# Kernel optimization log

Measured on AMD Instinct MI355X. Metric: run time of the kernel, lower is better.

## Reference

```python
import jax, jax.numpy as jnp
import numpy as np

K = 2            # top-k experts
SCALING = 16.0 / 16.0  # alpha / r


def setup_inputs() -> dict:
    key = jax.random.key(0)
    ks = jax.random.split(key, 7)
    B, T, D, O, E, R = 2, 4096, 2048, 2048, 8, 16
    return {
        "x": jax.random.normal(ks[0], (B, T, D), dtype=jnp.float32),
        "W": jax.random.normal(ks[1], (O, D), dtype=jnp.float32) * (1.0 / np.sqrt(D)),
        "b": jax.random.normal(ks[2], (O,), dtype=jnp.float32) * 0.02,
        "lora_A": jax.random.normal(ks[3], (E, R, D), dtype=jnp.float32) * (1.0 / np.sqrt(D)),
        "lora_B": jax.random.normal(ks[4], (E, O, R), dtype=jnp.float32) * 0.02,
        "gate_w": jax.random.normal(ks[5], (E, D), dtype=jnp.float32) * 0.02,
        "gate_b": jax.random.normal(ks[6], (E,), dtype=jnp.float32) * 0.02,
    }


def reference(x, W, b, lora_A, lora_B, gate_w, gate_b):
    orig_shape = x.shape
    D = orig_shape[-1]
    O = W.shape[0]
    x_flat = x.reshape(-1, D)                                  # [N, D]

    base = x_flat @ W.T + b                                    # [N, O]

    logits = x_flat @ gate_w.T + gate_b                        # [N, E] (eval: no noise)
    topk_logits, topk_idx = jax.lax.top_k(logits, K)           # [N, K]
    gates = jax.nn.softmax(topk_logits, axis=-1)               # [N, K]

    xA = jnp.einsum('nd,erd->ner', x_flat, lora_A)             # [N, E, R]
    delta_all = jnp.einsum('ner,eor->neo', xA, lora_B)         # [N, E, O]

    delta_topk = jnp.take_along_axis(delta_all, topk_idx[:, :, None], axis=1)  # [N, K, O]
    lora_update = jnp.sum(delta_topk * gates[:, :, None], axis=1)              # [N, O]

    out = base + SCALING * lora_update
    return out.reshape(*orig_shape[:-1], O)
```

## Files before the change

kernel.cpp:

```cpp
#include <hip/hip_runtime.h>
#include <hip/hip_bf16.h>
#include <stdint.h>

#define N_ROWS 8192
#define DIM    2048
#define OUTD   2048
#define NEXP   8
#define RNK    16
#define ZCOLS  128
#define KAUG   2176
#define KSPLIT 4
#define KSLICE (DIM / KSPLIT)

typedef unsigned short u16;
typedef float  f32x4  __attribute__((ext_vector_type(4)));
typedef __bf16 bf16x8 __attribute__((ext_vector_type(8)));

__device__ __forceinline__ u16 f2bf(float f) {
  unsigned u = __float_as_uint(f);
  return (u16)((u + 0x7fffu + ((u >> 16) & 1u)) >> 16);
}

__global__ __launch_bounds__(256) void k1_convert_gate(
    const float* __restrict__ x, const float* __restrict__ gw,
    const float* __restrict__ gb, u16* __restrict__ xaug,
    int* __restrict__ sel, float* __restrict__ gv)
{
  const int wave = threadIdx.x >> 6;
  const int lane = threadIdx.x & 63;
  const int row0 = blockIdx.x * 8 + wave * 2;

  float xv[2][32];
  #pragma unroll
  for (int rr = 0; rr < 2; ++rr) {
    const float* xr = x + (size_t)(row0 + rr) * DIM;
    #pragma unroll
    for (int i = 0; i < 8; ++i) {
      float4 v = *(const float4*)(xr + (lane * 4 + i * 256));
      xv[rr][i*4+0] = v.x; xv[rr][i*4+1] = v.y;
      xv[rr][i*4+2] = v.z; xv[rr][i*4+3] = v.w;
    }
  }
  #pragma unroll
  for (int rr = 0; rr < 2; ++rr) {
    u16* dst = xaug + (size_t)(row0 + rr) * KAUG;
    #pragma unroll
    for (int i = 0; i < 8; ++i) {
      ushort4 s;
      s.x = f2bf(xv[rr][i*4+0]); s.y = f2bf(xv[rr][i*4+1]);
      s.z = f2bf(xv[rr][i*4+2]); s.w = f2bf(xv[rr][i*4+3]);
      *(ushort4*)(dst + (lane * 4 + i * 256)) = s;
    }
  }
  float lg[2][NEXP];
  #pragma unroll
  for (int e = 0; e < NEXP; ++e) {
    const float* ge = gw + (size_t)e * DIM;
    float s0 = 0.f, s1 = 0.f;
    #pragma unroll
    for (int i = 0; i < 8; ++i) {
      float4 g4 = *(const float4*)(ge + (lane * 4 + i * 256));
      s0 += xv[0][i*4+0]*g4.x + xv[0][i*4+1]*g4.y + xv[0][i*4+2]*g4.z + xv[0][i*4+3]*g4.w;
      s1 += xv[1][i*4+0]*g4.x + xv[1][i*4+1]*g4.y + xv[1][i*4+2]*g4.z + xv[1][i*4+3]*g4.w;
    }
    #pragma unroll
    for (int off = 32; off > 0; off >>= 1) {
      s0 += __shfl_xor(s0, off);
      s1 += __shfl_xor(s1, off);
    }
    lg[0][e] = s0 + gb[e];
    lg[1][e] = s1 + gb[e];
  }
  if (lane == 0) {
    #pragma unroll
    for (int rr = 0; rr < 2; ++rr) {
      int e0 = 0; float m0 = lg[rr][0];
      #pragma unroll
      for (int e = 1; e < NEXP; ++e) if (lg[rr][e] > m0) { m0 = lg[rr][e]; e0 = e; }
      int e1 = (e0 == 0) ? 1 : 0; float m1 = lg[rr][e1];
      #pragma unroll
      for (int e = 0; e < NEXP; ++e) if (e != e0 && lg[rr][e] > m1) { m1 = lg[rr][e]; e1 = e; }
      float t   = expf(m1 - m0);
      float inv = 1.f / (1.f + t);
      int r = row0 + rr;
      sel[2*r] = e0; sel[2*r+1] = e1;
      gv[2*r]  = inv; gv[2*r+1] = t * inv;
    }
  }
}

__global__ __launch_bounds__(256) void k2_weights(
    const float* __restrict__ W, const float* __restrict__ lB,
    const float* __restrict__ lA, u16* __restrict__ waug, u16* __restrict__ ab)
{
  const int t = threadIdx.x;
  const int bid = blockIdx.x;
  if (bid < OUTD) {
    const int o = bid;
    const float* wr = W + (size_t)o * DIM;
    u16* dst = waug + (size_t)o * KAUG;
    #pragma unroll
    for (int i = 0; i < 2; ++i) {
      int c = t * 4 + i * 1024;
      float4 v = *(const float4*)(wr + c);
      ushort4 s; s.x = f2bf(v.x); s.y = f2bf(v.y); s.z = f2bf(v.z); s.w = f2bf(v.w);
      *(ushort4*)(dst + c) = s;
    }
    if (t < ZCOLS) {
      int e = t >> 4, r = t & 15;
      dst[DIM + t] = f2bf(lB[((size_t)e * OUTD + o) * RNK + r]);
    }
  } else {
    const int ar = bid - OUTD;
    const float* src = lA + (size_t)ar * DIM;
    u16* dst = ab + (size_t)ar * DIM;
    #pragma unroll
    for (int i = 0; i < 2; ++i) {
      int c = t * 4 + i * 1024;
      float4 v = *(const float4*)(src + c);
      ushort4 s; s.x = f2bf(v.x); s.y = f2bf(v.y); s.z = f2bf(v.z); s.w = f2bf(v.w);
      *(ushort4*)(dst + c) = s;
    }
  }
}

template <int BM, int BN, int BK, int WM, int WN, int MF, int NF>
__global__ __launch_bounds__(WM*WN*64) void gemm_ksplit(
    const u16* __restrict__ A, int lda,
    const u16* __restrict__ Bm, int ldb,
    int Ksz, int gm, float* __restrict__ outP)
{
  static_assert(BM == WM * MF * 16 && BN == WN * NF * 16 && BK == 64, "geom");
  constexpr int NW   = WM * WN;
  constexpr int ROWB = BK * 2;
  __shared__ __align__(16) u16 As[2][BM * BK];
  __shared__ __align__(16) u16 Bs[2][BN * BK];

  const int wave = threadIdx.x >> 6;
  const int lane = threadIdx.x & 63;

  int bid = blockIdx.x;
  const int nwg = gridDim.x;
  if ((nwg & 7) == 0) {
    const int cpx = nwg >> 3;
    bid = (bid & 7) * cpx + (bid >> 3);
  }
  const int tm  = bid % gm;
  const int ksl = bid / gm;
  const size_t row0 = (size_t)tm * BM;
  const u16* Ak = A  + (size_t)ksl * Ksz;
  const u16* Bk = Bm + (size_t)ksl * Ksz;

  auto stage = [&](const u16* __restrict__ g, int ld, size_t r0, int k0,
                   u16* lds, int nrows) {
    const int nch = nrows * (ROWB / 16);
    for (int c0 = wave * 64; c0 < nch; c0 += NW * 64) {
      const int c   = c0 + lane;
      const int r   = c >> 3;
      const int ch  = c & 7;
      const int sch = ch ^ (r & 7);
      const char* src = (const char*)(g + (r0 + (size_t)r) * ld + k0) + (sch << 4);
      __builtin_amdgcn_global_load_lds(
          (__attribute__((address_space(1))) void*)src,
          (__attribute__((address_space(3))) void*)((char*)lds + ((size_t)c0 << 4)),
          16, 0, 0);
    }
  };

  const int wm = wave / WN, wn = wave % WN;
  const int aRow = wm * MF * 16 + (lane & 15);
  const int bRow = wn * NF * 16 + (lane & 15);
  const int kq   = (lane >> 4) << 4;

  f32x4 acc[MF][NF] = {};

  const int nk = Ksz / BK;
  stage(Ak, lda, row0, 0, As[0], BM);
  stage(Bk, ldb, 0,    0, Bs[0], BN);
  __syncthreads();

  for (int t = 0; t < nk; ++t) {
    const int cur = t & 1;
    if (t + 1 < nk) {
      stage(Ak, lda, row0, (t + 1) * BK, As[cur ^ 1], BM);
      stage(Bk, ldb, 0,    (t + 1) * BK, Bs[cur ^ 1], BN);
    }
    const char* ab_ = (const char*)As[cur];
    const char* bb_ = (const char*)Bs[cur];
    #pragma unroll
    for (int ks = 0; ks < BK / 32; ++ks) {
      bf16x8 av[MF], bv[NF];
      #pragma unroll
      for (int mf = 0; mf < MF; ++mf) {
        const int r  = aRow + mf * 16;
        const int bo = (ks * 64 + kq) ^ ((r & 7) << 4);
        av[mf] = *(const bf16x8*)(ab_ + r * ROWB + bo);
      }
      #pragma unroll
      for (int nf = 0; nf < NF; ++nf) {
        const int r  = bRow + nf * 16;
        const int bo = (ks * 64 + kq) ^ ((r & 7) << 4);
        bv[nf] = *(const bf16x8*)(bb_ + r * ROWB + bo);
      }
      #pragma unroll
      for (int mf = 0; mf < MF; ++mf)
        #pragma unroll
        for (int nf = 0; nf < NF; ++nf)
          acc[mf][nf] = __builtin_amdgcn_mfma_f32_16x16x32_bf16(
              av[mf], bv[nf], acc[mf][nf], 0, 0, 0);
    }
    __syncthreads();
  }

  float* op = outP + (size_t)ksl * N_ROWS * ZCOLS;
  #pragma unroll
  for (int nf = 0; nf < NF; ++nf) {
    const int c = wn * NF * 16 + nf * 16 + (lane & 15);
    #pragma unroll
    for (int mf = 0; mf < MF; ++mf) {
      const size_t rb = row0 + wm * MF * 16 + mf * 16 + ((lane >> 4) << 2);
      #pragma unroll
      for (int j = 0; j < 4; ++j)
        op[(rb + j) * ZCOLS + c] = acc[mf][nf][j];
    }
  }
}

__global__ __launch_bounds__(256) void k3b_reduce_gate(
    const float* __restrict__ zpart, const int* __restrict__ sel,
    const float* __restrict__ gv, u16* __restrict__ xaug)
{
  const int idx = blockIdx.x * 256 + threadIdx.x;
  const int row = idx >> 5;
  const int c4  = (idx & 31) << 2;
  const float* zr = zpart + (size_t)row * ZCOLS + c4;
  const size_t sl = (size_t)N_ROWS * ZCOLS;
  float4 s = *(const float4*)zr;
  #pragma unroll
  for (int k = 1; k < KSPLIT; ++k) {
    float4 v = *(const float4*)(zr + k * sl);
    s.x += v.x; s.y += v.y; s.z += v.z; s.w += v.w;
  }
  const int e  = c4 >> 4;
  const int e0 = sel[2 * row], e1 = sel[2 * row + 1];
  const float g = (e == e0) ? gv[2 * row] : ((e == e1) ? gv[2 * row + 1] : 0.f);
  ushort4 o;
  o.x = f2bf(s.x * g); o.y = f2bf(s.y * g);
  o.z = f2bf(s.z * g); o.w = f2bf(s.w * g);
  *(ushort4*)(xaug + (size_t)row * KAUG + DIM + c4) = o;
}

__global__ __launch_bounds__(512, 2) void gemm256_pipe(
    const u16* __restrict__ A, int lda,
    const u16* __restrict__ Bm, int ldb,
    int Ksz, int grid_n,
    float* __restrict__ outF, int ldo, const float* __restrict__ bias)
{
  __shared__ __align__(16) u16 smem[65536];

  const int tid  = threadIdx.x;
  const int wave = tid >> 6;
  const int lane = tid & 63;

  int bid = blockIdx.x;
  const int nwg = gridDim.x;
  if ((nwg & 7) == 0) {
    const int cpx = nwg >> 3;
    bid = (bid & 7) * cpx + (bid >> 3);
  }
  const int tm = bid / grid_n;
  const int tn = bid % grid_n;
  const size_t row0 = (size_t)tm * 256;
  const size_t col0 = (size_t)tn * 256;

  const int l3  = lane >> 3;
  const int sch = ((lane & 7) ^ l3) << 4;
  const char* aSrc = (const char*)(A  + (row0 + (size_t)(wave * 8 + l3)) * lda) + sch;
  const char* bSrc = (const char*)(Bm + (col0 + (size_t)(wave * 8 + l3)) * ldb) + sch;
  const size_t arst = (size_t)lda * 128;
  const size_t brst = (size_t)ldb * 128;
  char* ldsA = (char*)smem + wave * 1024;
  char* ldsB = (char*)smem + 65536 + wave * 1024;

  auto stage = [&](int tt) {
    const size_t ko = (size_t)tt * 128;
    const int    sb = (tt & 1) << 15;
    #pragma unroll
    for (int i = 0; i < 4; ++i)
      __builtin_amdgcn_global_load_lds(
          (__attribute__((address_space(1))) void*)(aSrc + ko + i * arst),
          (__attribute__((address_space(3))) void*)(ldsA + sb + i * 8192), 16, 0, 0);
    #pragma unroll
    for (int i = 0; i < 4; ++i)
      __builtin_amdgcn_global_load_lds(
          (__attribute__((address_space(1))) void*)(bSrc + ko + i * brst),
          (__attribute__((address_space(3))) void*)(ldsB + sb + i * 8192), 16, 0, 0);
  };

  const int wm = wave >> 2, wn = wave & 3;
  const int x0 = ((lane >> 4) ^ (lane & 7)) << 4;
  const int offA0 = wm * 16384 + (lane & 15) * 128 + x0;
  const int offB0 = wn * 8192  + (lane & 15) * 128 + x0;

  f32x4 acc[8][4] = {};

  const int nk = Ksz / 64;
  stage(0); stage(1);

  for (int t = 0; t < nk; ++t) {
    if (t + 1 < nk) asm volatile("s_waitcnt vmcnt(8)" ::: "memory");
    else            asm volatile("s_waitcnt vmcnt(0)" ::: "memory");
    __builtin_amdgcn_s_barrier();
    __builtin_amdgcn_sched_barrier(0);

    const char* sa = (const char*)smem + ((t & 1) << 15);
    const char* sb = (const char*)smem + 65536 + ((t & 1) << 15);

    bf16x8 av[8], bv[4];
    #pragma unroll
    for (int mf = 0; mf < 8; ++mf) av[mf] = *(const bf16x8*)(sa + offA0 + mf * 2048);
    #pragma unroll
    for (int nf = 0; nf < 4; ++nf) bv[nf] = *(const bf16x8*)(sb + offB0 + nf * 2048);
    __builtin_amdgcn_s_setprio(1);
    #pragma unroll
    for (int mf = 0; mf < 8; ++mf)
      #pragma unroll
      for (int nf = 0; nf < 4; ++nf)
        acc[mf][nf] = __builtin_amdgcn_mfma_f32_16x16x32_bf16(
            av[mf], bv[nf], acc[mf][nf], 0, 0, 0);
    __builtin_amdgcn_s_setprio(0);

    #pragma unroll
    for (int mf = 0; mf < 8; ++mf) av[mf] = *(const bf16x8*)(sa + (offA0 ^ 64) + mf * 2048);
    #pragma unroll
    for (int nf = 0; nf < 4; ++nf) bv[nf] = *(const bf16x8*)(sb + (offB0 ^ 64) + nf * 2048);
    asm volatile("s_waitcnt lgkmcnt(0)" ::: "memory");
    __builtin_amdgcn_s_barrier();
    __builtin_amdgcn_sched_barrier(0);
    if (t + 2 < nk) stage(t + 2);
    __builtin_amdgcn_s_setprio(1);
    #pragma unroll
    for (int mf = 0; mf < 8; ++mf)
      #pragma unroll
      for (int nf = 0; nf < 4; ++nf)
        acc[mf][nf] = __builtin_amdgcn_mfma_f32_16x16x32_bf16(
            av[mf], bv[nf], acc[mf][nf], 0, 0, 0);
    __builtin_amdgcn_s_setprio(0);
  }

  #pragma unroll
  for (int nf = 0; nf < 4; ++nf) {
    const size_t c = col0 + wn * 64 + nf * 16 + (lane & 15);
    const float bvv = bias[c];
    #pragma unroll
    for (int mf = 0; mf < 8; ++mf) {
      const size_t rb = row0 + wm * 128 + mf * 16 + ((lane >> 4) << 2);
      #pragma unroll
      for (int j = 0; j < 4; ++j)
        outF[(rb + j) * (size_t)ldo + c] = acc[mf][nf][j] + bvv;
    }
  }
}

extern "C" void kernel_launch(void* const* d_in, const int* in_sizes, int n_in,
                              void* d_out, int out_size, void* d_ws, size_t ws_size,
                              hipStream_t stream) {
  const float* x  = (const float*)d_in[0];
  const float* W  = (const float*)d_in[1];
  const float* b  = (const float*)d_in[2];
  const float* lA = (const float*)d_in[3];
  const float* lB = (const float*)d_in[4];
  const float* gw = (const float*)d_in[5];
  const float* gb = (const float*)d_in[6];
  float* out = (float*)d_out;

  u16*   xaug  = (u16*)d_ws;
  u16*   waug  = xaug + (size_t)N_ROWS * KAUG;
  u16*   ab    = waug + (size_t)OUTD * KAUG;
  int*   sel   = (int*)(ab + (size_t)ZCOLS * DIM);
  float* gv    = (float*)(sel + 2 * N_ROWS);
  float* zpart = (float*)(gv + 2 * N_ROWS);

  hipLaunchKernelGGL(k1_convert_gate, dim3(N_ROWS / 8), dim3(256), 0, stream,
                     x, gw, gb, xaug, sel, gv);
  hipLaunchKernelGGL(k2_weights, dim3(OUTD + ZCOLS), dim3(256), 0, stream,
                     W, lB, lA, waug, ab);
  hipLaunchKernelGGL((gemm_ksplit<128, 128, 64, 2, 2, 4, 4>),
                     dim3((N_ROWS / 128) * KSPLIT), dim3(256), 0, stream,
                     xaug, KAUG, ab, DIM, KSLICE, N_ROWS / 128, zpart);
  hipLaunchKernelGGL(k3b_reduce_gate, dim3(N_ROWS * 32 / 256), dim3(256), 0, stream,
                     zpart, sel, gv, xaug);
  hipLaunchKernelGGL(gemm256_pipe,
                     dim3((N_ROWS / 256) * (OUTD / 256)), dim3(512), 0, stream,
                     xaug, KAUG, waug, KAUG, KAUG, OUTD / 256,
                     out, OUTD, b);
}
```

Measured before the change: 126.3 us.

## Fuse conversion, gating, LoRA-A projection and gate scaling into one kernel

Replaces the separate convert/gate kernel, the split-K LoRA-A GEMM and the reduce/gate kernel with one fused kernel. Each block handles 16 rows, streams x and gate weights, writes bf16 x, computes the gate logits and the x·A projection with MFMA, then writes the gated z columns directly. This removes two launches and the zpart partial-sum round trip through global memory, and x is no longer read again from the bf16 copy for the projection. The main GEMM's inner loop is also reordered to interleave the second set of LDS loads with half of the first set of MFMAs. The trade-off is that each fused block re-streams the whole lora_A matrix, with small per-block MFMA work.

```diff
diff --git a/kernel.cpp b/kernel.cpp
--- a/kernel.cpp
+++ b/kernel.cpp
@@ -9,8 +9,6 @@
 #define RNK    16
 #define ZCOLS  128
 #define KAUG   2176
-#define KSPLIT 4
-#define KSLICE (DIM / KSPLIT)
 
 typedef unsigned short u16;
 typedef float  f32x4  __attribute__((ext_vector_type(4)));
@@ -19,74 +17,6 @@
 __device__ __forceinline__ u16 f2bf(float f) {
   unsigned u = __float_as_uint(f);
   return (u16)((u + 0x7fffu + ((u >> 16) & 1u)) >> 16);
-}
-
-__global__ __launch_bounds__(256) void k1_convert_gate(
-    const float* __restrict__ x, const float* __restrict__ gw,
-    const float* __restrict__ gb, u16* __restrict__ xaug,
-    int* __restrict__ sel, float* __restrict__ gv)
-{
-  const int wave = threadIdx.x >> 6;
-  const int lane = threadIdx.x & 63;
-  const int row0 = blockIdx.x * 8 + wave * 2;
-
-  float xv[2][32];
-  #pragma unroll
-  for (int rr = 0; rr < 2; ++rr) {
-    const float* xr = x + (size_t)(row0 + rr) * DIM;
-    #pragma unroll
-    for (int i = 0; i < 8; ++i) {
-      float4 v = *(const float4*)(xr + (lane * 4 + i * 256));
-      xv[rr][i*4+0] = v.x; xv[rr][i*4+1] = v.y;
-      xv[rr][i*4+2] = v.z; xv[rr][i*4+3] = v.w;
-    }
-  }
-  #pragma unroll
-  for (int rr = 0; rr < 2; ++rr) {
-    u16* dst = xaug + (size_t)(row0 + rr) * KAUG;
-    #pragma unroll
-    for (int i = 0; i < 8; ++i) {
-      ushort4 s;
-      s.x = f2bf(xv[rr][i*4+0]); s.y = f2bf(xv[rr][i*4+1]);
-      s.z = f2bf(xv[rr][i*4+2]); s.w = f2bf(xv[rr][i*4+3]);
-      *(ushort4*)(dst + (lane * 4 + i * 256)) = s;
-    }
-  }
-  float lg[2][NEXP];
-  #pragma unroll
-  for (int e = 0; e < NEXP; ++e) {
-    const float* ge = gw + (size_t)e * DIM;
-    float s0 = 0.f, s1 = 0.f;
-    #pragma unroll
-    for (int i = 0; i < 8; ++i) {
-      float4 g4 = *(const float4*)(ge + (lane * 4 + i * 256));
-      s0 += xv[0][i*4+0]*g4.x + xv[0][i*4+1]*g4.y + xv[0][i*4+2]*g4.z + xv[0][i*4+3]*g4.w;
-      s1 += xv[1][i*4+0]*g4.x + xv[1][i*4+1]*g4.y + xv[1][i*4+2]*g4.z + xv[1][i*4+3]*g4.w;
-    }
-    #pragma unroll
-    for (int off = 32; off > 0; off >>= 1) {
-      s0 += __shfl_xor(s0, off);
-      s1 += __shfl_xor(s1, off);
-    }
-    lg[0][e] = s0 + gb[e];
-    lg[1][e] = s1 + gb[e];
-  }
-  if (lane == 0) {
-    #pragma unroll
-    for (int rr = 0; rr < 2; ++rr) {
-      int e0 = 0; float m0 = lg[rr][0];
-      #pragma unroll
-      for (int e = 1; e < NEXP; ++e) if (lg[rr][e] > m0) { m0 = lg[rr][e]; e0 = e; }
-      int e1 = (e0 == 0) ? 1 : 0; float m1 = lg[rr][e1];
-      #pragma unroll
-      for (int e = 0; e < NEXP; ++e) if (e != e0 && lg[rr][e] > m1) { m1 = lg[rr][e]; e1 = e; }
-      float t   = expf(m1 - m0);
-      float inv = 1.f / (1.f + t);
-      int r = row0 + rr;
-      sel[2*r] = e0; sel[2*r+1] = e1;
-      gv[2*r]  = inv; gv[2*r+1] = t * inv;
-    }
-  }
 }
 
 __global__ __launch_bounds__(256) void k2_weights(
@@ -124,130 +54,127 @@
   }
 }
 
-template <int BM, int BN, int BK, int WM, int WN, int MF, int NF>
-__global__ __launch_bounds__(WM*WN*64) void gemm_ksplit(
-    const u16* __restrict__ A, int lda,
-    const u16* __restrict__ Bm, int ldb,
-    int Ksz, int gm, float* __restrict__ outP)
+__global__ __launch_bounds__(256) void kf_fused(
+    const float* __restrict__ x, const float* __restrict__ gw,
+    const float* __restrict__ gb, const u16* __restrict__ ab,
+    u16* __restrict__ xaug)
 {
-  static_assert(BM == WM * MF * 16 && BN == WN * NF * 16 && BK == 64, "geom");
-  constexpr int NW   = WM * WN;
-  constexpr int ROWB = BK * 2;
-  __shared__ __align__(16) u16 As[2][BM * BK];
-  __shared__ __align__(16) u16 Bs[2][BN * BK];
-
-  const int wave = threadIdx.x >> 6;
-  const int lane = threadIdx.x & 63;
-
-  int bid = blockIdx.x;
-  const int nwg = gridDim.x;
-  if ((nwg & 7) == 0) {
-    const int cpx = nwg >> 3;
-    bid = (bid & 7) * cpx + (bid >> 3);
-  }
-  const int tm  = bid % gm;
-  const int ksl = bid / gm;
-  const size_t row0 = (size_t)tm * BM;
-  const u16* Ak = A  + (size_t)ksl * Ksz;
-  const u16* Bk = Bm + (size_t)ksl * Ksz;
-
-  auto stage = [&](const u16* __restrict__ g, int ld, size_t r0, int k0,
-                   u16* lds, int nrows) {
-    const int nch = nrows * (ROWB / 16);
-    for (int c0 = wave * 64; c0 < nch; c0 += NW * 64) {
-      const int c   = c0 + lane;
-      const int r   = c >> 3;
-      const int ch  = c & 7;
-      const int sch = ch ^ (r & 7);
-      const char* src = (const char*)(g + (r0 + (size_t)r) * ld + k0) + (sch << 4);
+  __shared__ __align__(16) u16 la[8192];
+  __shared__ __align__(16) u16 xb[1024];
+  __shared__ float4 gates[16];
+
+  const int t    = threadIdx.x;
+  const int wave = t >> 6;
+  const int lane = t & 63;
+  const int r    = t >> 4;
+  const int q    = t & 15;
+  const size_t row0 = (size_t)blockIdx.x * 16;
+
+  int   lrow[4], lsch[4];
+  #pragma unroll
+  for (int i = 0; i < 4; ++i) {
+    const int g = t + i * 256;
+    lrow[i] = g >> 3;
+    lsch[i] = (g & 7) ^ (lrow[i] & 7);
+  }
+
+  float4 xv, gwv[8];
+  xv = *(const float4*)(x + (row0 + r) * DIM + q * 4);
+  #pragma unroll
+  for (int e = 0; e < NEXP; ++e)
+    gwv[e] = *(const float4*)(gw + (size_t)e * DIM + q * 4);
+
+  float ga[NEXP] = {};
+  f32x4 acc[2] = {};
+  const int nfA = 2 * wave, nfB = 2 * wave + 1;
+
+  for (int c = 0; c < 32; ++c) {
+    const int C0 = c * 64;
+    #pragma unroll
+    for (int i = 0; i < 4; ++i) {
+      const char* src = (const char*)(ab + (size_t)lrow[i] * DIM + C0 + lsch[i] * 8);
       __builtin_amdgcn_global_load_lds(
           (__attribute__((address_space(1))) void*)src,
-          (__attribute__((address_space(3))) void*)((char*)lds + ((size_t)c0 << 4)),
+          (__attribute__((address_space(3))) void*)((char*)la + (wave * 64 + i * 256) * 16),
           16, 0, 0);
     }
-  };
-
-  const int wm = wave / WN, wn = wave % WN;
-  const int aRow = wm * MF * 16 + (lane & 15);
-  const int bRow = wn * NF * 16 + (lane & 15);
-  const int kq   = (lane >> 4) << 4;
-
-  f32x4 acc[MF][NF] = {};
-
-  const int nk = Ksz / BK;
-  stage(Ak, lda, row0, 0, As[0], BM);
-  stage(Bk, ldb, 0,    0, Bs[0], BN);
+    __builtin_amdgcn_sched_barrier(0);
+    float4 xvn, gwvn[8];
+    if (c + 1 < 32) {
+      xvn = *(const float4*)(x + (row0 + r) * DIM + C0 + 64 + q * 4);
+      #pragma unroll
+      for (int e = 0; e < NEXP; ++e)
+        gwvn[e] = *(const float4*)(gw + (size_t)e * DIM + C0 + 64 + q * 4);
+    }
+    __builtin_amdgcn_sched_barrier(0);
+    ushort4 s; s.x = f2bf(xv.x); s.y = f2bf(xv.y); s.z = f2bf(xv.z); s.w = f2bf(xv.w);
+    *(ushort4*)(xaug + (row0 + r) * KAUG + C0 + q * 4) = s;
+    #pragma unroll
+    for (int e = 0; e < NEXP; ++e)
+      ga[e] += xv.x * gwv[e].x + xv.y * gwv[e].y + xv.z * gwv[e].z + xv.w * gwv[e].w;
+    {
+      const int ch = q >> 1;
+      const int by = r * 128 + ((ch ^ (r & 7)) * 16) + (q & 1) * 8;
+      *(ushort4*)((char*)xb + by) = s;
+    }
+    if (c + 1 < 32) asm volatile("s_waitcnt vmcnt(9)" ::: "memory");
+    else            asm volatile("s_waitcnt vmcnt(0)" ::: "memory");
+    asm volatile("s_waitcnt lgkmcnt(0)" ::: "memory");
+    __builtin_amdgcn_s_barrier();
+
+    #pragma unroll
+    for (int ks = 0; ks < 2; ++ks) {
+      const int ra  = lane & 15;
+      const int pa  = ((ks * 4 + (lane >> 4)) ^ (ra & 7)) * 16;
+      bf16x8 avf = *(const bf16x8*)((char*)xb + ra * 128 + pa);
+      const int rbA = (lane & 15) + 16 * nfA;
+      const int rbB = (lane & 15) + 16 * nfB;
+      bf16x8 bvA = *(const bf16x8*)((char*)la + rbA * 128 + (((ks * 4 + (lane >> 4)) ^ (rbA & 7)) * 16));
+      bf16x8 bvB = *(const bf16x8*)((char*)la + rbB * 128 + (((ks * 4 + (lane >> 4)) ^ (rbB & 7)) * 16));
+      acc[0] = __builtin_amdgcn_mfma_f32_16x16x32_bf16(avf, bvA, acc[0], 0, 0, 0);
+      acc[1] = __builtin_amdgcn_mfma_f32_16x16x32_bf16(avf, bvB, acc[1], 0, 0, 0);
+    }
+    __builtin_amdgcn_s_barrier();
+    xv = xvn;
+    #pragma unroll
+    for (int e = 0; e < NEXP; ++e) gwv[e] = gwvn[e];
+  }
+
+  #pragma unroll
+  for (int e = 0; e < NEXP; ++e) {
+    float v = ga[e];
+    v += __shfl_xor(v, 1); v += __shfl_xor(v, 2);
+    v += __shfl_xor(v, 4); v += __shfl_xor(v, 8);
+    ga[e] = v + gb[e];
+  }
+  if (q == 0) {
+    int e0 = 0; float m0 = ga[0];
+    #pragma unroll
+    for (int e = 1; e < NEXP; ++e) if (ga[e] > m0) { m0 = ga[e]; e0 = e; }
+    int e1 = (e0 == 0) ? 1 : 0; float m1 = ga[e1];
+    #pragma unroll
+    for (int e = 0; e < NEXP; ++e) if (e != e0 && ga[e] > m1) { m1 = ga[e]; e1 = e; }
+    float tt  = expf(m1 - m0);
+    float inv = 1.f / (1.f + tt);
+    float4 gg; gg.x = inv; gg.y = tt * inv;
+    gg.z = __int_as_float(e0); gg.w = __int_as_float(e1);
+    gates[r] = gg;
+  }
   __syncthreads();
 
-  for (int t = 0; t < nk; ++t) {
-    const int cur = t & 1;
-    if (t + 1 < nk) {
-      stage(Ak, lda, row0, (t + 1) * BK, As[cur ^ 1], BM);
-      stage(Bk, ldb, 0,    (t + 1) * BK, Bs[cur ^ 1], BN);
-    }
-    const char* ab_ = (const char*)As[cur];
-    const char* bb_ = (const char*)Bs[cur];
-    #pragma unroll
-    for (int ks = 0; ks < BK / 32; ++ks) {
-      bf16x8 av[MF], bv[NF];
-      #pragma unroll
-      for (int mf = 0; mf < MF; ++mf) {
-        const int r  = aRow + mf * 16;
-        const int bo = (ks * 64 + kq) ^ ((r & 7) << 4);
-        av[mf] = *(const bf16x8*)(ab_ + r * ROWB + bo);
-      }
-      #pragma unroll
-      for (int nf = 0; nf < NF; ++nf) {
-        const int r  = bRow + nf * 16;
-        const int bo = (ks * 64 + kq) ^ ((r & 7) << 4);
-        bv[nf] = *(const bf16x8*)(bb_ + r * ROWB + bo);
-      }
-      #pragma unroll
-      for (int mf = 0; mf < MF; ++mf)
-        #pragma unroll
-        for (int nf = 0; nf < NF; ++nf)
-          acc[mf][nf] = __builtin_amdgcn_mfma_f32_16x16x32_bf16(
-              av[mf], bv[nf], acc[mf][nf], 0, 0, 0);
-    }
-    __syncthreads();
-  }
-
-  float* op = outP + (size_t)ksl * N_ROWS * ZCOLS;
-  #pragma unroll
-  for (int nf = 0; nf < NF; ++nf) {
-    const int c = wn * NF * 16 + nf * 16 + (lane & 15);
-    #pragma unroll
-    for (int mf = 0; mf < MF; ++mf) {
-      const size_t rb = row0 + wm * MF * 16 + mf * 16 + ((lane >> 4) << 2);
-      #pragma unroll
-      for (int j = 0; j < 4; ++j)
-        op[(rb + j) * ZCOLS + c] = acc[mf][nf][j];
-    }
-  }
-}
-
-__global__ __launch_bounds__(256) void k3b_reduce_gate(
-    const float* __restrict__ zpart, const int* __restrict__ sel,
-    const float* __restrict__ gv, u16* __restrict__ xaug)
-{
-  const int idx = blockIdx.x * 256 + threadIdx.x;
-  const int row = idx >> 5;
-  const int c4  = (idx & 31) << 2;
-  const float* zr = zpart + (size_t)row * ZCOLS + c4;
-  const size_t sl = (size_t)N_ROWS * ZCOLS;
-  float4 s = *(const float4*)zr;
-  #pragma unroll
-  for (int k = 1; k < KSPLIT; ++k) {
-    float4 v = *(const float4*)(zr + k * sl);
-    s.x += v.x; s.y += v.y; s.z += v.z; s.w += v.w;
-  }
-  const int e  = c4 >> 4;
-  const int e0 = sel[2 * row], e1 = sel[2 * row + 1];
-  const float g = (e == e0) ? gv[2 * row] : ((e == e1) ? gv[2 * row + 1] : 0.f);
-  ushort4 o;
-  o.x = f2bf(s.x * g); o.y = f2bf(s.y * g);
-  o.z = f2bf(s.z * g); o.w = f2bf(s.w * g);
-  *(ushort4*)(xaug + (size_t)row * KAUG + DIM + c4) = o;
+  #pragma unroll
+  for (int nfl = 0; nfl < 2; ++nfl) {
+    const int e = 2 * wave + nfl;
+    const int n = e * 16 + (lane & 15);
+    #pragma unroll
+    for (int j = 0; j < 4; ++j) {
+      const int m = (lane >> 4) * 4 + j;
+      float4 gg = gates[m];
+      const float g = (e == __float_as_int(gg.z)) ? gg.x
+                    : ((e == __float_as_int(gg.w)) ? gg.y : 0.f);
+      xaug[(row0 + m) * KAUG + DIM + n] = f2bf(acc[nfl][j] * g);
+    }
+  }
 }
 
 __global__ __launch_bounds__(512, 2) void gemm256_pipe(
@@ -316,24 +243,31 @@
     const char* sa = (const char*)smem + ((t & 1) << 15);
     const char* sb = (const char*)smem + 65536 + ((t & 1) << 15);
 
-    bf16x8 av[8], bv[4];
-    #pragma unroll
-    for (int mf = 0; mf < 8; ++mf) av[mf] = *(const bf16x8*)(sa + offA0 + mf * 2048);
-    #pragma unroll
-    for (int nf = 0; nf < 4; ++nf) bv[nf] = *(const bf16x8*)(sb + offB0 + nf * 2048);
+    bf16x8 av0[8], bv0[4], av1[8], bv1[4];
+    #pragma unroll
+    for (int mf = 0; mf < 8; ++mf) av0[mf] = *(const bf16x8*)(sa + offA0 + mf * 2048);
+    #pragma unroll
+    for (int nf = 0; nf < 4; ++nf) bv0[nf] = *(const bf16x8*)(sb + offB0 + nf * 2048);
     __builtin_amdgcn_s_setprio(1);
     #pragma unroll
     for (int mf = 0; mf < 8; ++mf)
       #pragma unroll
-      for (int nf = 0; nf < 4; ++nf)
+      for (int nf = 0; nf < 2; ++nf)
         acc[mf][nf] = __builtin_amdgcn_mfma_f32_16x16x32_bf16(
-            av[mf], bv[nf], acc[mf][nf], 0, 0, 0);
+            av0[mf], bv0[nf], acc[mf][nf], 0, 0, 0);
     __builtin_amdgcn_s_setprio(0);
-
-    #pragma unroll
-    for (int mf = 0; mf < 8; ++mf) av[mf] = *(const bf16x8*)(sa + (offA0 ^ 64) + mf * 2048);
-    #pragma unroll
-    for (int nf = 0; nf < 4; ++nf) bv[nf] = *(const bf16x8*)(sb + (offB0 ^ 64) + nf * 2048);
+    #pragma unroll
+    for (int mf = 0; mf < 8; ++mf) av1[mf] = *(const bf16x8*)(sa + (offA0 ^ 64) + mf * 2048);
+    #pragma unroll
+    for (int nf = 0; nf < 4; ++nf) bv1[nf] = *(const bf16x8*)(sb + (offB0 ^ 64) + nf * 2048);
+    __builtin_amdgcn_s_setprio(1);
+    #pragma unroll
+    for (int mf = 0; mf < 8; ++mf)
+      #pragma unroll
+      for (int nf = 2; nf < 4; ++nf)
+        acc[mf][nf] = __builtin_amdgcn_mfma_f32_16x16x32_bf16(
+            av0[mf], bv0[nf], acc[mf][nf], 0, 0, 0);
+    __builtin_amdgcn_s_setprio(0);
     asm volatile("s_waitcnt lgkmcnt(0)" ::: "memory");
     __builtin_amdgcn_s_barrier();
     __builtin_amdgcn_sched_barrier(0);
@@ -344,7 +278,7 @@
       #pragma unroll
       for (int nf = 0; nf < 4; ++nf)
         acc[mf][nf] = __builtin_amdgcn_mfma_f32_16x16x32_bf16(
-            av[mf], bv[nf], acc[mf][nf], 0, 0, 0);
+            av1[mf], bv1[nf], acc[mf][nf], 0, 0, 0);
     __builtin_amdgcn_s_setprio(0);
   }
 
@@ -374,22 +308,14 @@
   const float* gb = (const float*)d_in[6];
   float* out = (float*)d_out;
 
-  u16*   xaug  = (u16*)d_ws;
-  u16*   waug  = xaug + (size_t)N_ROWS * KAUG;
-  u16*   ab    = waug + (size_t)OUTD * KAUG;
-  int*   sel   = (int*)(ab + (size_t)ZCOLS * DIM);
-  float* gv    = (float*)(sel + 2 * N_ROWS);
-  float* zpart = (float*)(gv + 2 * N_ROWS);
-
-  hipLaunchKernelGGL(k1_convert_gate, dim3(N_ROWS / 8), dim3(256), 0, stream,
-                     x, gw, gb, xaug, sel, gv);
+  u16* xaug = (u16*)d_ws;
+  u16* waug = xaug + (size_t)N_ROWS * KAUG;
+  u16* ab   = waug + (size_t)OUTD * KAUG;
+
   hipLaunchKernelGGL(k2_weights, dim3(OUTD + ZCOLS), dim3(256), 0, stream,
                      W, lB, lA, waug, ab);
-  hipLaunchKernelGGL((gemm_ksplit<128, 128, 64, 2, 2, 4, 4>),
-                     dim3((N_ROWS / 128) * KSPLIT), dim3(256), 0, stream,
-                     xaug, KAUG, ab, DIM, KSLICE, N_ROWS / 128, zpart);
-  hipLaunchKernelGGL(k3b_reduce_gate, dim3(N_ROWS * 32 / 256), dim3(256), 0, stream,
-                     zpart, sel, gv, xaug);
+  hipLaunchKernelGGL(kf_fused, dim3(N_ROWS / 16), dim3(256), 0, stream,
+                     x, gw, gb, ab, xaug);
   hipLaunchKernelGGL(gemm256_pipe,
                      dim3((N_ROWS / 256) * (OUTD / 256)), dim3(512), 0, stream,
                      xaug, KAUG, waug, KAUG, KAUG, OUTD / 256,
```

New measurement: 120.7 us. -4.4%, faster.
